# Performance work log

Measured on AMD Instinct MI355X. Metric: run time of the kernel, lower is better.

The kernel has to match this reference:

```python
import jax, jax.numpy as jnp
import numpy as np


def setup_inputs() -> dict:
    key = jax.random.key(0)
    ks = jax.random.split(key, 5)
    B, L, C = 32, 64, 128      # batch, set_size, input_channels
    D, O = 512, 256            # mlp hidden dim, output_channels
    L2 = L * L                 # 4096 = set_size**2 (FSPool set size)
    x = jax.random.normal(ks[0], (B, L, C), dtype=jnp.float32)
    # Linear weights stored as [in, out]; kaiming-ish scaling
    w1 = jax.random.normal(ks[1], (2 * C, D), dtype=jnp.float32) / np.sqrt(2 * C)
    b1 = jnp.zeros((D,), dtype=jnp.float32)
    w2 = jax.random.normal(ks[2], (D, O), dtype=jnp.float32) / np.sqrt(D)
    b2 = jnp.zeros((O,), dtype=jnp.float32)
    # FSPool weight [set_size**2, out_channels], kaiming_normal fan_out linear
    pool_w = jax.random.normal(ks[3], (L2, O), dtype=jnp.float32) / np.sqrt(O)
    return {"x": x, "w1": w1, "b1": b1, "w2": w2, "b2": b2, "pool_w": pool_w}


def reference(x, w1, b1, w2, b2, pool_w):
    B, L, C = x.shape
    # create_pairs + concat: [B, L, L, 2C] -> flatten to [B, L*L, 2C]
    a = jnp.broadcast_to(x[:, :, None, :], (B, L, L, C))
    b = jnp.broadcast_to(x[:, None, :, :], (B, L, L, C))
    pairs = jnp.concatenate([a, b], axis=-1).reshape(B, L * L, 2 * C)
    # 2-layer MLP
    h = jax.nn.relu(pairs @ w1 + b1)            # [B, L^2, D]
    y = h @ w2 + b2                             # [B, L^2, O]
    # FSPool: featurewise sort over set dim, then weighted sum
    y = jnp.sort(y, axis=1)                     # [B, L^2, O]
    return jnp.einsum('nlc,lc->nc', y, pool_w)  # [B, O]
```

## Files before the change

kernel.cpp:

```cpp
#include <hip/hip_runtime.h>
#include <hip/hip_bf16.h>
#include <hip/hip_fp16.h>

typedef __attribute__((ext_vector_type(4))) float f32x4;
typedef _Float16 h8 __attribute__((ext_vector_type(8)));
typedef int i32x4 __attribute__((ext_vector_type(4)));
typedef _Float16 h2 __attribute__((ext_vector_type(2)));

static __device__ __forceinline__ h2 ih2(int x) { return __builtin_bit_cast(h2, x); }
static __device__ __forceinline__ unsigned pkrtz(float lo, float hi) {
  return __builtin_bit_cast(unsigned, __builtin_amdgcn_cvt_pkrtz(lo, hi));
}
static __device__ __forceinline__ int pkmin(int x, int y) {
  int d; asm("v_pk_min_f16 %0, %1, %2" : "=v"(d) : "v"(x), "v"(y)); return d;
}
static __device__ __forceinline__ int pkmax(int x, int y) {
  int d; asm("v_pk_max_f16 %0, %1, %2" : "=v"(d) : "v"(x), "v"(y)); return d;
}
static __device__ __forceinline__ int pkadd(int x, int y) {
  int d; asm("v_pk_add_f16 %0, %1, %2" : "=v"(d) : "v"(x), "v"(y)); return d;
}


__global__ __launch_bounds__(256) void k_uv(const float* __restrict__ x,
                                            const float* __restrict__ w1,
                                            const float* __restrict__ b1,
                                            _Float16* __restrict__ u,
                                            _Float16* __restrict__ v) {
  __shared__ float xs[8 * 128];
  int t = threadIdx.x;
  int r0 = blockIdx.x * 8;
  ((float4*)xs)[t] = ((const float4*)(x + (size_t)r0 * 128))[t];
  __syncthreads();
  int d1 = t, d2 = t + 256;
  float au0[8], au1[8], av0[8], av1[8];
  float bb1 = b1[d1], bb2 = b1[d2];
#pragma unroll
  for (int r = 0; r < 8; ++r) { au0[r] = bb1; au1[r] = bb2; av0[r] = 0.f; av1[r] = 0.f; }
#pragma unroll 4
  for (int c = 0; c < 128; ++c) {
    float wu1 = w1[c * 512 + d1];
    float wu2 = w1[c * 512 + d2];
    float wv1 = w1[(c + 128) * 512 + d1];
    float wv2 = w1[(c + 128) * 512 + d2];
#pragma unroll
    for (int r = 0; r < 8; ++r) {
      float xv = xs[r * 128 + c];
      au0[r] = fmaf(xv, wu1, au0[r]);
      au1[r] = fmaf(xv, wu2, au1[r]);
      av0[r] = fmaf(xv, wv1, av0[r]);
      av1[r] = fmaf(xv, wv2, av1[r]);
    }
  }
#pragma unroll
  for (int r = 0; r < 8; ++r) {
    u[(size_t)(r0 + r) * 512 + d1] = (_Float16)au0[r];
    u[(size_t)(r0 + r) * 512 + d2] = (_Float16)au1[r];
    v[(size_t)(r0 + r) * 512 + d1] = (_Float16)av0[r];
    v[(size_t)(r0 + r) * 512 + d2] = (_Float16)av1[r];
  }
}

__global__ __launch_bounds__(256) void k_w2t(const float* __restrict__ w2,
                                             _Float16* __restrict__ w2t) {
  int n = blockIdx.x;
  int t = threadIdx.x;
  w2t[(size_t)n * 512 + t]       = (_Float16)w2[(size_t)t * 256 + n];
  w2t[(size_t)n * 512 + t + 256] = (_Float16)w2[(size_t)(t + 256) * 256 + n];
}

__global__ __launch_bounds__(256) void k_pwt(const float* __restrict__ pw,
                                             float* __restrict__ pwt) {
  int o = blockIdx.x;
  int t = threadIdx.x;
#pragma unroll
  for (int it = 0; it < 16; ++it) {
    int l = it * 256 + t;
    pwt[(size_t)o * 4096 + l] = pw[(size_t)l * 256 + o];
  }
}

__global__ __launch_bounds__(256, 2) void k_gemm(const _Float16* __restrict__ u,
                                                 const _Float16* __restrict__ v,
                                                 const _Float16* __restrict__ w2t,
                                                 const float* __restrict__ b2,
                                                 unsigned short* __restrict__ yt) {
  __shared__ char vl[64 * 1024];
  __shared__ char ulm[4 * 1024];
  int t = threadIdx.x;
  int n0 = blockIdx.x;
  int bid = (n0 & 7) * 64 + (n0 >> 3);
  int b = bid >> 4, ig = bid & 15;
  {
    const char* vsrc = (const char*)(v + (size_t)b * 64 * 512);
#pragma unroll
    for (int it = 0; it < 16; ++it) {
      int f = it * 4096 + t * 16;
      uint4 d = *(const uint4*)(vsrc + f);
      int row = f >> 10;
      *(uint4*)(vl + (f ^ ((row & 7) << 4))) = d;
    }
    const char* usrc = (const char*)(u + (size_t)(b * 64 + ig * 4) * 512);
    int f = t * 16;
    *(uint4*)(ulm + f) = *(const uint4*)(usrc + f);
  }
  __syncthreads();
  int w = t >> 6, l = t & 63, lr = l & 15, lg = l >> 4;
  const _Float16* bptr[4];
  float bias[4];
#pragma unroll
  for (int ni = 0; ni < 4; ++ni) {
    int col = w * 64 + ni * 16 + lr;
    bptr[ni] = w2t + (size_t)col * 512 + lg * 8;
    bias[ni] = b2[col];
  }
#pragma unroll 1
  for (int ih = 0; ih < 2; ++ih) {
    f32x4 acc[2][4][4];
#pragma unroll
    for (int ip = 0; ip < 2; ++ip)
#pragma unroll
      for (int mi = 0; mi < 4; ++mi)
#pragma unroll
        for (int ni = 0; ni < 4; ++ni) {
          float bv = bias[ni];
          f32x4 ci = {bv, bv, bv, bv};
          acc[ip][mi][ni] = ci;
        }
#pragma unroll 2
    for (int kk = 0; kk < 16; ++kk) {
      h8 bfv[4];
#pragma unroll
      for (int ni = 0; ni < 4; ++ni) bfv[ni] = *(const h8*)(bptr[ni] + kk * 32);
      i32x4 vf[4];
#pragma unroll
      for (int mi = 0; mi < 4; ++mi) {
        int row = mi * 16 + lr;
        int fb = row * 1024 + kk * 64 + lg * 16;
        vf[mi] = *(const i32x4*)(vl + (fb ^ ((row & 7) << 4)));
      }
#pragma unroll
      for (int ip = 0; ip < 2; ++ip) {
        i32x4 uf = *(const i32x4*)(ulm + (ih * 2 + ip) * 1024 + kk * 64 + lg * 16);
#pragma unroll
        for (int mi = 0; mi < 4; ++mi) {
          i32x4 aw;
#pragma unroll
          for (int q = 0; q < 4; ++q) aw[q] = pkmax(pkadd(uf[q], vf[mi][q]), 0);
          h8 af = __builtin_bit_cast(h8, aw);
#pragma unroll
          for (int ni = 0; ni < 4; ++ni)
            acc[ip][mi][ni] =
                __builtin_amdgcn_mfma_f32_16x16x32_f16(af, bfv[ni], acc[ip][mi][ni], 0, 0, 0);
        }
      }
    }
#pragma unroll
    for (int ip = 0; ip < 2; ++ip) {
      int i = ig * 4 + ih * 2 + ip;
#pragma unroll
      for (int ni = 0; ni < 4; ++ni) {
        int col = w * 64 + ni * 16 + lr;
        unsigned short* colbase = yt + (size_t)(b * 256 + col) * 4096 + (size_t)i * 64;
#pragma unroll
        for (int mi = 0; mi < 4; ++mi) {
          f32x4 vv = acc[ip][mi][ni];
          uint2 st;
          st.x = pkrtz(vv[0], vv[1]);
          st.y = pkrtz(vv[2], vv[3]);
          *(uint2*)(colbase + mi * 16 + lg * 4) = st;
        }
      }
    }
  }
}

#define DPP_X1 0xB1
#define DPP_X2 0x4E
#define DPP_X3 0x1B
#define DPP_X7 0x141
#define DPP_X8 0x128
#define DPP_XF 0x140

template <int M, int HB>
static __device__ __forceinline__ void intra(int* a) {
#pragma unroll
  for (int e = 0; e < 64; ++e)
    if ((e & HB) == 0) {
      int f = e ^ M;
      int lo = pkmin(a[e], a[f]);
      int hi = pkmax(a[e], a[f]);
      a[e] = lo;
      a[f] = hi;
    }
}

template <int CTRL>
static __device__ __forceinline__ void cdpp(int* a, bool km) {
#pragma unroll
  for (int e = 0; e < 64; ++e) {
    int r = __builtin_amdgcn_mov_dpp(a[e], CTRL, 0xf, 0xf, true);
    int mn = pkmin(a[e], r), mx = pkmax(a[e], r);
    a[e] = km ? mn : mx;
  }
}

template <int CTRL>
static __device__ __forceinline__ void fdpp(int* a, bool km) {
#pragma unroll
  for (int e = 0; e < 32; ++e) {
    int f = e ^ 63;
    int r0 = __builtin_amdgcn_mov_dpp(a[f], CTRL, 0xf, 0xf, true);
    int r1 = __builtin_amdgcn_mov_dpp(a[e], CTRL, 0xf, 0xf, true);
    int mn0 = pkmin(a[e], r0), mx0 = pkmax(a[e], r0);
    int mn1 = pkmin(a[f], r1), mx1 = pkmax(a[f], r1);
    a[e] = km ? mn0 : mx0;
    a[f] = km ? mn1 : mx1;
  }
}

static __device__ __forceinline__ void cbp(int* a, int tm, bool km, int l) {
  int paddr = ((l ^ tm) & 63) << 2;
#pragma unroll
  for (int e = 0; e < 64; ++e) {
    int r = __builtin_amdgcn_ds_bpermute(paddr, a[e]);
    int mn = pkmin(a[e], r), mx = pkmax(a[e], r);
    a[e] = km ? mn : mx;
  }
}

static __device__ __forceinline__ void fbp(int* a, int tm, bool km, int l) {
  int paddr = ((l ^ tm) & 63) << 2;
#pragma unroll
  for (int e = 0; e < 32; ++e) {
    int f = e ^ 63;
    int r0 = __builtin_amdgcn_ds_bpermute(paddr, a[f]);
    int r1 = __builtin_amdgcn_ds_bpermute(paddr, a[e]);
    int mn0 = pkmin(a[e], r0), mx0 = pkmax(a[e], r0);
    int mn1 = pkmin(a[f], r1), mx1 = pkmax(a[f], r1);
    a[e] = km ? mn0 : mx0;
    a[f] = km ? mn1 : mx1;
  }
}

__global__ __launch_bounds__(64, 2) void k_sortpool(const unsigned short* __restrict__ yt,
                                                    const float* __restrict__ pwt,
                                                    float* __restrict__ out) {
  int t = threadIdx.x;
  int b = blockIdx.x >> 7, p = blockIdx.x & 127;
  int o0 = p * 2, o1 = o0 + 1;
  const uint4* c0 = (const uint4*)(yt + (size_t)(b * 256 + o0) * 4096 + t * 64);
  const uint4* c1 = (const uint4*)(yt + (size_t)(b * 256 + o1) * 4096 + t * 64);
  int a[64];
#pragma unroll
  for (int q = 0; q < 8; ++q) {
    uint4 x0 = c0[q], x1 = c1[q];
    unsigned w0[4] = {x0.x, x0.y, x0.z, x0.w};
    unsigned w1[4] = {x1.x, x1.y, x1.z, x1.w};
#pragma unroll
    for (int r = 0; r < 4; ++r) {
      a[q * 8 + 2 * r]     = (int)((w0[r] & 0xffffu) | (w1[r] << 16));
      a[q * 8 + 2 * r + 1] = (int)((w0[r] >> 16) | (w1[r] & 0xffff0000u));
    }
  }
  intra<1, 1>(a);
  intra<3, 2>(a); intra<1, 1>(a);
  intra<7, 4>(a); intra<2, 2>(a); intra<1, 1>(a);
  intra<15, 8>(a); intra<4, 4>(a); intra<2, 2>(a); intra<1, 1>(a);
  intra<31, 16>(a); intra<8, 8>(a); intra<4, 4>(a); intra<2, 2>(a); intra<1, 1>(a);
  intra<63, 32>(a); intra<16, 16>(a); intra<8, 8>(a); intra<4, 4>(a);
  intra<2, 2>(a); intra<1, 1>(a);
#define CLEAN6 intra<32, 32>(a); intra<16, 16>(a); intra<8, 8>(a); \
               intra<4, 4>(a); intra<2, 2>(a); intra<1, 1>(a)
  fdpp<DPP_X1>(a, !(t & 1)); CLEAN6;
  fdpp<DPP_X3>(a, !(t & 2)); cdpp<DPP_X1>(a, !(t & 1)); CLEAN6;
  fdpp<DPP_X7>(a, !(t & 4)); cdpp<DPP_X2>(a, !(t & 2)); cdpp<DPP_X1>(a, !(t & 1)); CLEAN6;
  fdpp<DPP_XF>(a, !(t & 8)); cbp(a, 4, !(t & 4), t);
  cdpp<DPP_X2>(a, !(t & 2)); cdpp<DPP_X1>(a, !(t & 1)); CLEAN6;
  fbp(a, 31, !(t & 16), t); cdpp<DPP_X8>(a, !(t & 8)); cbp(a, 4, !(t & 4), t);
  cdpp<DPP_X2>(a, !(t & 2)); cdpp<DPP_X1>(a, !(t & 1)); CLEAN6;
  fbp(a, 63, !(t & 32), t); cbp(a, 16, !(t & 16), t); cdpp<DPP_X8>(a, !(t & 8));
  cbp(a, 4, !(t & 4), t); cdpp<DPP_X2>(a, !(t & 2)); cdpp<DPP_X1>(a, !(t & 1)); CLEAN6;
#undef CLEAN6
  const float4* pw0 = (const float4*)(pwt + (size_t)o0 * 4096 + t * 64);
  const float4* pw1 = (const float4*)(pwt + (size_t)o1 * 4096 + t * 64);
  float s0 = 0.f, s1 = 0.f;
#pragma unroll
  for (int q = 0; q < 16; ++q) {
    float4 w0 = pw0[q], w1 = pw1[q];
    float k0[4] = {w0.x, w0.y, w0.z, w0.w};
    float k1[4] = {w1.x, w1.y, w1.z, w1.w};
#pragma unroll
    for (int r = 0; r < 4; ++r) {
      h2 v2 = ih2(a[q * 4 + r]);
      s0 = fmaf((float)v2[0], k0[r], s0);
      s1 = fmaf((float)v2[1], k1[r], s1);
    }
  }
#pragma unroll
  for (int off = 32; off > 0; off >>= 1) {
    s0 += __shfl_xor(s0, off);
    s1 += __shfl_xor(s1, off);
  }
  if (t == 0) {
    out[b * 256 + o0] = s0;
    out[b * 256 + o1] = s1;
  }
}

extern "C" void kernel_launch(void* const* d_in, const int* in_sizes, int n_in,
                              void* d_out, int out_size, void* d_ws, size_t ws_size,
                              hipStream_t stream) {
  const float* x  = (const float*)d_in[0];
  const float* w1 = (const float*)d_in[1];
  const float* b1 = (const float*)d_in[2];
  const float* w2 = (const float*)d_in[3];
  const float* b2 = (const float*)d_in[4];
  const float* pw = (const float*)d_in[5];
  char* ws = (char*)d_ws;
  _Float16* u   = (_Float16*)ws;
  _Float16* v   = (_Float16*)(ws + (2u << 20));
  _Float16* w2t = (_Float16*)(ws + (4u << 20));
  float*    pwt = (float*)(ws + (5u << 20));
  unsigned short* yt = (unsigned short*)(ws + (9u << 20));
  float* out = (float*)d_out;

  k_uv<<<dim3(256), dim3(256), 0, stream>>>(x, w1, b1, u, v);
  k_w2t<<<dim3(256), dim3(256), 0, stream>>>(w2, w2t);
  k_pwt<<<dim3(256), dim3(256), 0, stream>>>(pw, pwt);
  k_gemm<<<dim3(512), dim3(256), 0, stream>>>(u, v, w2t, b2, yt);
  k_sortpool<<<dim3(4096), dim3(64), 0, stream>>>(yt, pwt, out);
}
```

Baseline: 153.3 us.

## Merge prep kernels and cut compare-exchange instruction count in bitonic sort

Folds the three preprocessing kernels (uv projection, w2 transpose, pool-weight transpose) into a single launch that dispatches on block index, removing two kernel launches. The in-register bitonic sort now does each compare-exchange with an xor/max/xor trick (three ops, no separate min) and keeps the cross-lane result with v_bfi on a precomputed lane mask instead of a min, a max and a select. The sortpool launch-bounds min-blocks hint is dropped. Correctness depends on the xor trick and the bfi masks selecting the right halves.

```diff
diff --git a/kernel.cpp b/kernel.cpp
--- a/kernel.cpp
+++ b/kernel.cpp
@@ -11,72 +11,85 @@
 static __device__ __forceinline__ unsigned pkrtz(float lo, float hi) {
   return __builtin_bit_cast(unsigned, __builtin_amdgcn_cvt_pkrtz(lo, hi));
 }
-static __device__ __forceinline__ int pkmin(int x, int y) {
-  int d; asm("v_pk_min_f16 %0, %1, %2" : "=v"(d) : "v"(x), "v"(y)); return d;
-}
-static __device__ __forceinline__ int pkmax(int x, int y) {
+static __device__ __forceinline__ int pkmax_(int x, int y) {
   int d; asm("v_pk_max_f16 %0, %1, %2" : "=v"(d) : "v"(x), "v"(y)); return d;
 }
-static __device__ __forceinline__ int pkadd(int x, int y) {
+static __device__ __forceinline__ int pkadd_(int x, int y) {
   int d; asm("v_pk_add_f16 %0, %1, %2" : "=v"(d) : "v"(x), "v"(y)); return d;
 }
 
-
-__global__ __launch_bounds__(256) void k_uv(const float* __restrict__ x,
-                                            const float* __restrict__ w1,
-                                            const float* __restrict__ b1,
-                                            _Float16* __restrict__ u,
-                                            _Float16* __restrict__ v) {
+static __device__ __forceinline__ void ce(int& x, int& y) {
+  int t;
+  asm("v_xor_b32 %2, %0, %1\n\t"
+      "v_pk_max_f16 %1, %0, %1\n\t"
+      "v_xor_b32 %0, %2, %1"
+      : "+v"(x), "+v"(y), "=&v"(t));
+}
+
+static __device__ __forceinline__ void keep(int& a, int r, int msel) {
+  int mn;
+  asm("v_pk_min_f16 %1, %0, %2\n\t"
+      "v_pk_max_f16 %0, %0, %2\n\t"
+      "v_bfi_b32 %0, %3, %1, %0"
+      : "+v"(a), "=&v"(mn)
+      : "v"(r), "v"(msel));
+}
+
+
+__global__ __launch_bounds__(256) void k_prep(const float* __restrict__ x,
+                                              const float* __restrict__ w1,
+                                              const float* __restrict__ b1,
+                                              const float* __restrict__ w2,
+                                              const float* __restrict__ pw,
+                                              _Float16* __restrict__ u,
+                                              _Float16* __restrict__ v,
+                                              _Float16* __restrict__ w2t,
+                                              float* __restrict__ pwt) {
   __shared__ float xs[8 * 128];
+  int bid = blockIdx.x;
   int t = threadIdx.x;
-  int r0 = blockIdx.x * 8;
-  ((float4*)xs)[t] = ((const float4*)(x + (size_t)r0 * 128))[t];
-  __syncthreads();
-  int d1 = t, d2 = t + 256;
-  float au0[8], au1[8], av0[8], av1[8];
-  float bb1 = b1[d1], bb2 = b1[d2];
-#pragma unroll
-  for (int r = 0; r < 8; ++r) { au0[r] = bb1; au1[r] = bb2; av0[r] = 0.f; av1[r] = 0.f; }
+  if (bid < 256) {
+    int r0 = bid * 8;
+    ((float4*)xs)[t] = ((const float4*)(x + (size_t)r0 * 128))[t];
+    __syncthreads();
+    int d1 = t, d2 = t + 256;
+    float au0[8], au1[8], av0[8], av1[8];
+    float bb1 = b1[d1], bb2 = b1[d2];
+#pragma unroll
+    for (int r = 0; r < 8; ++r) { au0[r] = bb1; au1[r] = bb2; av0[r] = 0.f; av1[r] = 0.f; }
 #pragma unroll 4
-  for (int c = 0; c < 128; ++c) {
-    float wu1 = w1[c * 512 + d1];
-    float wu2 = w1[c * 512 + d2];
-    float wv1 = w1[(c + 128) * 512 + d1];
-    float wv2 = w1[(c + 128) * 512 + d2];
+    for (int c = 0; c < 128; ++c) {
+      float wu1 = w1[c * 512 + d1];
+      float wu2 = w1[c * 512 + d2];
+      float wv1 = w1[(c + 128) * 512 + d1];
+      float wv2 = w1[(c + 128) * 512 + d2];
+#pragma unroll
+      for (int r = 0; r < 8; ++r) {
+        float xv = xs[r * 128 + c];
+        au0[r] = fmaf(xv, wu1, au0[r]);
+        au1[r] = fmaf(xv, wu2, au1[r]);
+        av0[r] = fmaf(xv, wv1, av0[r]);
+        av1[r] = fmaf(xv, wv2, av1[r]);
+      }
+    }
 #pragma unroll
     for (int r = 0; r < 8; ++r) {
-      float xv = xs[r * 128 + c];
-      au0[r] = fmaf(xv, wu1, au0[r]);
-      au1[r] = fmaf(xv, wu2, au1[r]);
-      av0[r] = fmaf(xv, wv1, av0[r]);
-      av1[r] = fmaf(xv, wv2, av1[r]);
-    }
-  }
-#pragma unroll
-  for (int r = 0; r < 8; ++r) {
-    u[(size_t)(r0 + r) * 512 + d1] = (_Float16)au0[r];
-    u[(size_t)(r0 + r) * 512 + d2] = (_Float16)au1[r];
-    v[(size_t)(r0 + r) * 512 + d1] = (_Float16)av0[r];
-    v[(size_t)(r0 + r) * 512 + d2] = (_Float16)av1[r];
-  }
-}
-
-__global__ __launch_bounds__(256) void k_w2t(const float* __restrict__ w2,
-                                             _Float16* __restrict__ w2t) {
-  int n = blockIdx.x;
-  int t = threadIdx.x;
-  w2t[(size_t)n * 512 + t]       = (_Float16)w2[(size_t)t * 256 + n];
-  w2t[(size_t)n * 512 + t + 256] = (_Float16)w2[(size_t)(t + 256) * 256 + n];
-}
-
-__global__ __launch_bounds__(256) void k_pwt(const float* __restrict__ pw,
-                                             float* __restrict__ pwt) {
-  int o = blockIdx.x;
-  int t = threadIdx.x;
-#pragma unroll
-  for (int it = 0; it < 16; ++it) {
-    int l = it * 256 + t;
-    pwt[(size_t)o * 4096 + l] = pw[(size_t)l * 256 + o];
+      u[(size_t)(r0 + r) * 512 + d1] = (_Float16)au0[r];
+      u[(size_t)(r0 + r) * 512 + d2] = (_Float16)au1[r];
+      v[(size_t)(r0 + r) * 512 + d1] = (_Float16)av0[r];
+      v[(size_t)(r0 + r) * 512 + d2] = (_Float16)av1[r];
+    }
+  } else if (bid < 512) {
+    int n = bid - 256;
+    w2t[(size_t)n * 512 + t]       = (_Float16)w2[(size_t)t * 256 + n];
+    w2t[(size_t)n * 512 + t + 256] = (_Float16)w2[(size_t)(t + 256) * 256 + n];
+  } else {
+    int o = bid - 512;
+#pragma unroll
+    for (int it = 0; it < 16; ++it) {
+      int l = it * 256 + t;
+      pwt[(size_t)o * 4096 + l] = pw[(size_t)l * 256 + o];
+    }
   }
 }
 
@@ -146,7 +159,7 @@
         for (int mi = 0; mi < 4; ++mi) {
           i32x4 aw;
 #pragma unroll
-          for (int q = 0; q < 4; ++q) aw[q] = pkmax(pkadd(uf[q], vf[mi][q]), 0);
+          for (int q = 0; q < 4; ++q) aw[q] = pkmax_(pkadd_(uf[q], vf[mi][q]), 0);
           h8 af = __builtin_bit_cast(h8, aw);
 #pragma unroll
           for (int ni = 0; ni < 4; ++ni)
@@ -186,66 +199,54 @@
 static __device__ __forceinline__ void intra(int* a) {
 #pragma unroll
   for (int e = 0; e < 64; ++e)
-    if ((e & HB) == 0) {
-      int f = e ^ M;
-      int lo = pkmin(a[e], a[f]);
-      int hi = pkmax(a[e], a[f]);
-      a[e] = lo;
-      a[f] = hi;
-    }
+    if ((e & HB) == 0) ce(a[e], a[e ^ M]);
 }
 
 template <int CTRL>
-static __device__ __forceinline__ void cdpp(int* a, bool km) {
+static __device__ __forceinline__ void cdpp(int* a, int msel) {
 #pragma unroll
   for (int e = 0; e < 64; ++e) {
     int r = __builtin_amdgcn_mov_dpp(a[e], CTRL, 0xf, 0xf, true);
-    int mn = pkmin(a[e], r), mx = pkmax(a[e], r);
-    a[e] = km ? mn : mx;
+    keep(a[e], r, msel);
   }
 }
 
 template <int CTRL>
-static __device__ __forceinline__ void fdpp(int* a, bool km) {
+static __device__ __forceinline__ void fdpp(int* a, int msel) {
 #pragma unroll
   for (int e = 0; e < 32; ++e) {
     int f = e ^ 63;
     int r0 = __builtin_amdgcn_mov_dpp(a[f], CTRL, 0xf, 0xf, true);
     int r1 = __builtin_amdgcn_mov_dpp(a[e], CTRL, 0xf, 0xf, true);
-    int mn0 = pkmin(a[e], r0), mx0 = pkmax(a[e], r0);
-    int mn1 = pkmin(a[f], r1), mx1 = pkmax(a[f], r1);
-    a[e] = km ? mn0 : mx0;
-    a[f] = km ? mn1 : mx1;
-  }
-}
-
-static __device__ __forceinline__ void cbp(int* a, int tm, bool km, int l) {
+    keep(a[e], r0, msel);
+    keep(a[f], r1, msel);
+  }
+}
+
+static __device__ __forceinline__ void cbp(int* a, int tm, int msel, int l) {
   int paddr = ((l ^ tm) & 63) << 2;
 #pragma unroll
   for (int e = 0; e < 64; ++e) {
     int r = __builtin_amdgcn_ds_bpermute(paddr, a[e]);
-    int mn = pkmin(a[e], r), mx = pkmax(a[e], r);
-    a[e] = km ? mn : mx;
-  }
-}
-
-static __device__ __forceinline__ void fbp(int* a, int tm, bool km, int l) {
+    keep(a[e], r, msel);
+  }
+}
+
+static __device__ __forceinline__ void fbp(int* a, int tm, int msel, int l) {
   int paddr = ((l ^ tm) & 63) << 2;
 #pragma unroll
   for (int e = 0; e < 32; ++e) {
     int f = e ^ 63;
     int r0 = __builtin_amdgcn_ds_bpermute(paddr, a[f]);
     int r1 = __builtin_amdgcn_ds_bpermute(paddr, a[e]);
-    int mn0 = pkmin(a[e], r0), mx0 = pkmax(a[e], r0);
-    int mn1 = pkmin(a[f], r1), mx1 = pkmax(a[f], r1);
-    a[e] = km ? mn0 : mx0;
-    a[f] = km ? mn1 : mx1;
-  }
-}
-
-__global__ __launch_bounds__(64, 2) void k_sortpool(const unsigned short* __restrict__ yt,
-                                                    const float* __restrict__ pwt,
-                                                    float* __restrict__ out) {
+    keep(a[e], r0, msel);
+    keep(a[f], r1, msel);
+  }
+}
+
+__global__ __launch_bounds__(64) void k_sortpool(const unsigned short* __restrict__ yt,
+                                                 const float* __restrict__ pwt,
+                                                 float* __restrict__ out) {
   int t = threadIdx.x;
   int b = blockIdx.x >> 7, p = blockIdx.x & 127;
   int o0 = p * 2, o1 = o0 + 1;
@@ -263,6 +264,12 @@
       a[q * 8 + 2 * r + 1] = (int)((w0[r] >> 16) | (w1[r] & 0xffff0000u));
     }
   }
+  int m1  = (t & 1)  ? 0 : -1;
+  int m2  = (t & 2)  ? 0 : -1;
+  int m4  = (t & 4)  ? 0 : -1;
+  int m8  = (t & 8)  ? 0 : -1;
+  int m16 = (t & 16) ? 0 : -1;
+  int m32 = (t & 32) ? 0 : -1;
   intra<1, 1>(a);
   intra<3, 2>(a); intra<1, 1>(a);
   intra<7, 4>(a); intra<2, 2>(a); intra<1, 1>(a);
@@ -272,15 +279,15 @@
   intra<2, 2>(a); intra<1, 1>(a);
 #define CLEAN6 intra<32, 32>(a); intra<16, 16>(a); intra<8, 8>(a); \
                intra<4, 4>(a); intra<2, 2>(a); intra<1, 1>(a)
-  fdpp<DPP_X1>(a, !(t & 1)); CLEAN6;
-  fdpp<DPP_X3>(a, !(t & 2)); cdpp<DPP_X1>(a, !(t & 1)); CLEAN6;
-  fdpp<DPP_X7>(a, !(t & 4)); cdpp<DPP_X2>(a, !(t & 2)); cdpp<DPP_X1>(a, !(t & 1)); CLEAN6;
-  fdpp<DPP_XF>(a, !(t & 8)); cbp(a, 4, !(t & 4), t);
-  cdpp<DPP_X2>(a, !(t & 2)); cdpp<DPP_X1>(a, !(t & 1)); CLEAN6;
-  fbp(a, 31, !(t & 16), t); cdpp<DPP_X8>(a, !(t & 8)); cbp(a, 4, !(t & 4), t);
-  cdpp<DPP_X2>(a, !(t & 2)); cdpp<DPP_X1>(a, !(t & 1)); CLEAN6;
-  fbp(a, 63, !(t & 32), t); cbp(a, 16, !(t & 16), t); cdpp<DPP_X8>(a, !(t & 8));
-  cbp(a, 4, !(t & 4), t); cdpp<DPP_X2>(a, !(t & 2)); cdpp<DPP_X1>(a, !(t & 1)); CLEAN6;
+  fdpp<DPP_X1>(a, m1); CLEAN6;
+  fdpp<DPP_X3>(a, m2); cdpp<DPP_X1>(a, m1); CLEAN6;
+  fdpp<DPP_X7>(a, m4); cdpp<DPP_X2>(a, m2); cdpp<DPP_X1>(a, m1); CLEAN6;
+  fdpp<DPP_XF>(a, m8); cbp(a, 4, m4, t);
+  cdpp<DPP_X2>(a, m2); cdpp<DPP_X1>(a, m1); CLEAN6;
+  fbp(a, 31, m16, t); cdpp<DPP_X8>(a, m8); cbp(a, 4, m4, t);
+  cdpp<DPP_X2>(a, m2); cdpp<DPP_X1>(a, m1); CLEAN6;
+  fbp(a, 63, m32, t); cbp(a, 16, m16, t); cdpp<DPP_X8>(a, m8);
+  cbp(a, 4, m4, t); cdpp<DPP_X2>(a, m2); cdpp<DPP_X1>(a, m1); CLEAN6;
 #undef CLEAN6
   const float4* pw0 = (const float4*)(pwt + (size_t)o0 * 4096 + t * 64);
   const float4* pw1 = (const float4*)(pwt + (size_t)o1 * 4096 + t * 64);
@@ -325,9 +332,7 @@
   unsigned short* yt = (unsigned short*)(ws + (9u << 20));
   float* out = (float*)d_out;
 
-  k_uv<<<dim3(256), dim3(256), 0, stream>>>(x, w1, b1, u, v);
-  k_w2t<<<dim3(256), dim3(256), 0, stream>>>(w2, w2t);
-  k_pwt<<<dim3(256), dim3(256), 0, stream>>>(pw, pwt);
+  k_prep<<<dim3(768), dim3(256), 0, stream>>>(x, w1, b1, w2, pw, u, v, w2t, pwt);
   k_gemm<<<dim3(512), dim3(256), 0, stream>>>(u, v, w2t, b2, yt);
   k_sortpool<<<dim3(4096), dim3(64), 0, stream>>>(yt, pwt, out);
 }
```

Result: no change. 151.0 us (-1.6%).

## Merge prep kernels and split GEMM into one-row blocks with wider N tiles

Applied to the files above, without the earlier changes.

Fuses the three preprocessing kernels (u/v projection, w2 transpose, pool weight transpose) into one launch, dispatching on block index. Reworks the GEMM so each block handles a single i row: four waves split into 2 j-halves by 2 n-halves, each holding 2x8 MFMA tiles, with 2048 blocks instead of 512. This adds parallelism and removes two launches, at the cost of reloading the 64KB v tile from global memory four times as often. Also drops the occupancy hint of 2 from the sortpool launch bounds.

```diff
diff --git a/kernel.cpp b/kernel.cpp
--- a/kernel.cpp
+++ b/kernel.cpp
@@ -22,61 +22,60 @@
 }
 
 
-__global__ __launch_bounds__(256) void k_uv(const float* __restrict__ x,
-                                            const float* __restrict__ w1,
-                                            const float* __restrict__ b1,
-                                            _Float16* __restrict__ u,
-                                            _Float16* __restrict__ v) {
+__global__ __launch_bounds__(256) void k_prep(const float* __restrict__ x,
+                                              const float* __restrict__ w1,
+                                              const float* __restrict__ b1,
+                                              const float* __restrict__ w2,
+                                              const float* __restrict__ pw,
+                                              _Float16* __restrict__ u,
+                                              _Float16* __restrict__ v,
+                                              _Float16* __restrict__ w2t,
+                                              float* __restrict__ pwt) {
   __shared__ float xs[8 * 128];
+  int bid = blockIdx.x;
   int t = threadIdx.x;
-  int r0 = blockIdx.x * 8;
-  ((float4*)xs)[t] = ((const float4*)(x + (size_t)r0 * 128))[t];
-  __syncthreads();
-  int d1 = t, d2 = t + 256;
-  float au0[8], au1[8], av0[8], av1[8];
-  float bb1 = b1[d1], bb2 = b1[d2];
-#pragma unroll
-  for (int r = 0; r < 8; ++r) { au0[r] = bb1; au1[r] = bb2; av0[r] = 0.f; av1[r] = 0.f; }
+  if (bid < 256) {
+    int r0 = bid * 8;
+    ((float4*)xs)[t] = ((const float4*)(x + (size_t)r0 * 128))[t];
+    __syncthreads();
+    int d1 = t, d2 = t + 256;
+    float au0[8], au1[8], av0[8], av1[8];
+    float bb1 = b1[d1], bb2 = b1[d2];
+#pragma unroll
+    for (int r = 0; r < 8; ++r) { au0[r] = bb1; au1[r] = bb2; av0[r] = 0.f; av1[r] = 0.f; }
 #pragma unroll 4
-  for (int c = 0; c < 128; ++c) {
-    float wu1 = w1[c * 512 + d1];
-    float wu2 = w1[c * 512 + d2];
-    float wv1 = w1[(c + 128) * 512 + d1];
-    float wv2 = w1[(c + 128) * 512 + d2];
+    for (int c = 0; c < 128; ++c) {
+      float wu1 = w1[c * 512 + d1];
+      float wu2 = w1[c * 512 + d2];
+      float wv1 = w1[(c + 128) * 512 + d1];
+      float wv2 = w1[(c + 128) * 512 + d2];
+#pragma unroll
+      for (int r = 0; r < 8; ++r) {
+        float xv = xs[r * 128 + c];
+        au0[r] = fmaf(xv, wu1, au0[r]);
+        au1[r] = fmaf(xv, wu2, au1[r]);
+        av0[r] = fmaf(xv, wv1, av0[r]);
+        av1[r] = fmaf(xv, wv2, av1[r]);
+      }
+    }
 #pragma unroll
     for (int r = 0; r < 8; ++r) {
-      float xv = xs[r * 128 + c];
-      au0[r] = fmaf(xv, wu1, au0[r]);
-      au1[r] = fmaf(xv, wu2, au1[r]);
-      av0[r] = fmaf(xv, wv1, av0[r]);
-      av1[r] = fmaf(xv, wv2, av1[r]);
-    }
-  }
-#pragma unroll
-  for (int r = 0; r < 8; ++r) {
-    u[(size_t)(r0 + r) * 512 + d1] = (_Float16)au0[r];
-    u[(size_t)(r0 + r) * 512 + d2] = (_Float16)au1[r];
-    v[(size_t)(r0 + r) * 512 + d1] = (_Float16)av0[r];
-    v[(size_t)(r0 + r) * 512 + d2] = (_Float16)av1[r];
-  }
-}
-
-__global__ __launch_bounds__(256) void k_w2t(const float* __restrict__ w2,
-                                             _Float16* __restrict__ w2t) {
-  int n = blockIdx.x;
-  int t = threadIdx.x;
-  w2t[(size_t)n * 512 + t]       = (_Float16)w2[(size_t)t * 256 + n];
-  w2t[(size_t)n * 512 + t + 256] = (_Float16)w2[(size_t)(t + 256) * 256 + n];
-}
-
-__global__ __launch_bounds__(256) void k_pwt(const float* __restrict__ pw,
-                                             float* __restrict__ pwt) {
-  int o = blockIdx.x;
-  int t = threadIdx.x;
-#pragma unroll
-  for (int it = 0; it < 16; ++it) {
-    int l = it * 256 + t;
-    pwt[(size_t)o * 4096 + l] = pw[(size_t)l * 256 + o];
+      u[(size_t)(r0 + r) * 512 + d1] = (_Float16)au0[r];
+      u[(size_t)(r0 + r) * 512 + d2] = (_Float16)au1[r];
+      v[(size_t)(r0 + r) * 512 + d1] = (_Float16)av0[r];
+      v[(size_t)(r0 + r) * 512 + d2] = (_Float16)av1[r];
+    }
+  } else if (bid < 512) {
+    int n = bid - 256;
+    w2t[(size_t)n * 512 + t]       = (_Float16)w2[(size_t)t * 256 + n];
+    w2t[(size_t)n * 512 + t + 256] = (_Float16)w2[(size_t)(t + 256) * 256 + n];
+  } else {
+    int o = bid - 512;
+#pragma unroll
+    for (int it = 0; it < 16; ++it) {
+      int l = it * 256 + t;
+      pwt[(size_t)o * 4096 + l] = pw[(size_t)l * 256 + o];
+    }
   }
 }
 
@@ -86,11 +85,11 @@
                                                  const float* __restrict__ b2,
                                                  unsigned short* __restrict__ yt) {
   __shared__ char vl[64 * 1024];
-  __shared__ char ulm[4 * 1024];
+  __shared__ char ulm[1024];
   int t = threadIdx.x;
   int n0 = blockIdx.x;
-  int bid = (n0 & 7) * 64 + (n0 >> 3);
-  int b = bid >> 4, ig = bid & 15;
+  int bid = (n0 & 7) * 256 + (n0 >> 3);
+  int b = bid >> 6, i = bid & 63;
   {
     const char* vsrc = (const char*)(v + (size_t)b * 64 * 512);
 #pragma unroll
@@ -100,79 +99,61 @@
       int row = f >> 10;
       *(uint4*)(vl + (f ^ ((row & 7) << 4))) = d;
     }
-    const char* usrc = (const char*)(u + (size_t)(b * 64 + ig * 4) * 512);
-    int f = t * 16;
-    *(uint4*)(ulm + f) = *(const uint4*)(usrc + f);
+    if (t < 64) {
+      const char* usrc = (const char*)(u + (size_t)(b * 64 + i) * 512);
+      *(uint4*)(ulm + t * 16) = *(const uint4*)(usrc + t * 16);
+    }
   }
   __syncthreads();
   int w = t >> 6, l = t & 63, lr = l & 15, lg = l >> 4;
-  const _Float16* bptr[4];
-  float bias[4];
-#pragma unroll
-  for (int ni = 0; ni < 4; ++ni) {
-    int col = w * 64 + ni * 16 + lr;
+  int jh = w & 1, nh = w >> 1;
+  const _Float16* bptr[8];
+  f32x4 acc[2][8];
+#pragma unroll
+  for (int ni = 0; ni < 8; ++ni) {
+    int col = nh * 128 + ni * 16 + lr;
     bptr[ni] = w2t + (size_t)col * 512 + lg * 8;
-    bias[ni] = b2[col];
-  }
-#pragma unroll 1
-  for (int ih = 0; ih < 2; ++ih) {
-    f32x4 acc[2][4][4];
-#pragma unroll
-    for (int ip = 0; ip < 2; ++ip)
-#pragma unroll
-      for (int mi = 0; mi < 4; ++mi)
-#pragma unroll
-        for (int ni = 0; ni < 4; ++ni) {
-          float bv = bias[ni];
-          f32x4 ci = {bv, bv, bv, bv};
-          acc[ip][mi][ni] = ci;
-        }
-#pragma unroll 2
-    for (int kk = 0; kk < 16; ++kk) {
-      h8 bfv[4];
-#pragma unroll
-      for (int ni = 0; ni < 4; ++ni) bfv[ni] = *(const h8*)(bptr[ni] + kk * 32);
-      i32x4 vf[4];
-#pragma unroll
-      for (int mi = 0; mi < 4; ++mi) {
-        int row = mi * 16 + lr;
-        int fb = row * 1024 + kk * 64 + lg * 16;
-        vf[mi] = *(const i32x4*)(vl + (fb ^ ((row & 7) << 4)));
-      }
-#pragma unroll
-      for (int ip = 0; ip < 2; ++ip) {
-        i32x4 uf = *(const i32x4*)(ulm + (ih * 2 + ip) * 1024 + kk * 64 + lg * 16);
-#pragma unroll
-        for (int mi = 0; mi < 4; ++mi) {
-          i32x4 aw;
-#pragma unroll
-          for (int q = 0; q < 4; ++q) aw[q] = pkmax(pkadd(uf[q], vf[mi][q]), 0);
-          h8 af = __builtin_bit_cast(h8, aw);
-#pragma unroll
-          for (int ni = 0; ni < 4; ++ni)
-            acc[ip][mi][ni] =
-                __builtin_amdgcn_mfma_f32_16x16x32_f16(af, bfv[ni], acc[ip][mi][ni], 0, 0, 0);
-        }
-      }
-    }
-#pragma unroll
-    for (int ip = 0; ip < 2; ++ip) {
-      int i = ig * 4 + ih * 2 + ip;
-#pragma unroll
-      for (int ni = 0; ni < 4; ++ni) {
-        int col = w * 64 + ni * 16 + lr;
-        unsigned short* colbase = yt + (size_t)(b * 256 + col) * 4096 + (size_t)i * 64;
-#pragma unroll
-        for (int mi = 0; mi < 4; ++mi) {
-          f32x4 vv = acc[ip][mi][ni];
-          uint2 st;
-          st.x = pkrtz(vv[0], vv[1]);
-          st.y = pkrtz(vv[2], vv[3]);
-          *(uint2*)(colbase + mi * 16 + lg * 4) = st;
-        }
-      }
-    }
-  }
+    float bv = b2[col];
+    f32x4 ci = {bv, bv, bv, bv};
+    acc[0][ni] = ci;
+    acc[1][ni] = ci;
+  }
+#pragma unroll 4
+  for (int kk = 0; kk < 16; ++kk) {
+    h8 bfv[8];
+#pragma unroll
+    for (int ni = 0; ni < 8; ++ni) bfv[ni] = *(const h8*)(bptr[ni] + kk * 32);
+    i32x4 uf = *(const i32x4*)(ulm + kk * 64 + lg * 16);
+    h8 af[2];
+#pragma unroll
+    for (int mi = 0; mi < 2; ++mi) {
+      int row = jh * 32 + mi * 16 + lr;
+      int fb = row * 1024 + kk * 64 + lg * 16;
+      i32x4 vf = *(const i32x4*)(vl + (fb ^ ((row & 7) << 4)));
+      i32x4 aw;
+#pragma unroll
+      for (int q = 0; q < 4; ++q) aw[q] = pkmax(pkadd(uf[q], vf[q]), 0);
+      af[mi] = __builtin_bit_cast(h8, aw);
+    }
+#pragma unroll
+    for (int mi = 0; mi < 2; ++mi)
+#pragma unroll
+      for (int ni = 0; ni < 8; ++ni)
+        acc[mi][ni] = __builtin_amdgcn_mfma_f32_16x16x32_f16(af[mi], bfv[ni], acc[mi][ni], 0, 0, 0);
+  }
+#pragma unroll
+  for (int mi = 0; mi < 2; ++mi)
+#pragma unroll
+    for (int ni = 0; ni < 8; ++ni) {
+      int col = nh * 128 + ni * 16 + lr;
+      unsigned short* colbase =
+          yt + (size_t)(b * 256 + col) * 4096 + (size_t)i * 64 + jh * 32 + mi * 16 + lg * 4;
+      f32x4 vv = acc[mi][ni];
+      uint2 st;
+      st.x = pkrtz(vv[0], vv[1]);
+      st.y = pkrtz(vv[2], vv[3]);
+      *(uint2*)colbase = st;
+    }
 }
 
 #define DPP_X1 0xB1
@@ -243,9 +224,9 @@
   }
 }
 
-__global__ __launch_bounds__(64, 2) void k_sortpool(const unsigned short* __restrict__ yt,
-                                                    const float* __restrict__ pwt,
-                                                    float* __restrict__ out) {
+__global__ __launch_bounds__(64) void k_sortpool(const unsigned short* __restrict__ yt,
+                                                 const float* __restrict__ pwt,
+                                                 float* __restrict__ out) {
   int t = threadIdx.x;
   int b = blockIdx.x >> 7, p = blockIdx.x & 127;
   int o0 = p * 2, o1 = o0 + 1;
@@ -325,9 +306,7 @@
   unsigned short* yt = (unsigned short*)(ws + (9u << 20));
   float* out = (float*)d_out;
 
-  k_uv<<<dim3(256), dim3(256), 0, stream>>>(x, w1, b1, u, v);
-  k_w2t<<<dim3(256), dim3(256), 0, stream>>>(w2, w2t);
-  k_pwt<<<dim3(256), dim3(256), 0, stream>>>(pw, pwt);
-  k_gemm<<<dim3(512), dim3(256), 0, stream>>>(u, v, w2t, b2, yt);
+  k_prep<<<dim3(768), dim3(256), 0, stream>>>(x, w1, b1, w2, pw, u, v, w2t, pwt);
+  k_gemm<<<dim3(2048), dim3(256), 0, stream>>>(u, v, w2t, b2, yt);
   k_sortpool<<<dim3(4096), dim3(64), 0, stream>>>(yt, pwt, out);
 }
```

Measured after the change: 229.7 us. +49.8%, slower.

## Merge prep kernels into one launch and split GEMM tiles across j halves

Applied to the files above, without the earlier changes.

The three preprocessing kernels (u/v projection, w2 transpose, pool-weight transpose) are merged into one launch that dispatches on block index, removing two kernel launches and their serialization gaps. The GEMM grid doubles to 1024 blocks, each handling half of the 64 j-rows, so the v tile in LDS shrinks to 32 KB and the accumulator set halves. The aim is more blocks per CU and better occupancy, at the cost of loading w2t B-fragments twice as often overall. The sortpool launch bound drops its min-blocks hint, which loosens the register cap.

```diff
diff --git a/kernel.cpp b/kernel.cpp
--- a/kernel.cpp
+++ b/kernel.cpp
@@ -22,61 +22,60 @@
 }
 
 
-__global__ __launch_bounds__(256) void k_uv(const float* __restrict__ x,
-                                            const float* __restrict__ w1,
-                                            const float* __restrict__ b1,
-                                            _Float16* __restrict__ u,
-                                            _Float16* __restrict__ v) {
+__global__ __launch_bounds__(256) void k_prep(const float* __restrict__ x,
+                                              const float* __restrict__ w1,
+                                              const float* __restrict__ b1,
+                                              const float* __restrict__ w2,
+                                              const float* __restrict__ pw,
+                                              _Float16* __restrict__ u,
+                                              _Float16* __restrict__ v,
+                                              _Float16* __restrict__ w2t,
+                                              float* __restrict__ pwt) {
   __shared__ float xs[8 * 128];
+  int bid = blockIdx.x;
   int t = threadIdx.x;
-  int r0 = blockIdx.x * 8;
-  ((float4*)xs)[t] = ((const float4*)(x + (size_t)r0 * 128))[t];
-  __syncthreads();
-  int d1 = t, d2 = t + 256;
-  float au0[8], au1[8], av0[8], av1[8];
-  float bb1 = b1[d1], bb2 = b1[d2];
-#pragma unroll
-  for (int r = 0; r < 8; ++r) { au0[r] = bb1; au1[r] = bb2; av0[r] = 0.f; av1[r] = 0.f; }
+  if (bid < 256) {
+    int r0 = bid * 8;
+    ((float4*)xs)[t] = ((const float4*)(x + (size_t)r0 * 128))[t];
+    __syncthreads();
+    int d1 = t, d2 = t + 256;
+    float au0[8], au1[8], av0[8], av1[8];
+    float bb1 = b1[d1], bb2 = b1[d2];
+#pragma unroll
+    for (int r = 0; r < 8; ++r) { au0[r] = bb1; au1[r] = bb2; av0[r] = 0.f; av1[r] = 0.f; }
 #pragma unroll 4
-  for (int c = 0; c < 128; ++c) {
-    float wu1 = w1[c * 512 + d1];
-    float wu2 = w1[c * 512 + d2];
-    float wv1 = w1[(c + 128) * 512 + d1];
-    float wv2 = w1[(c + 128) * 512 + d2];
+    for (int c = 0; c < 128; ++c) {
+      float wu1 = w1[c * 512 + d1];
+      float wu2 = w1[c * 512 + d2];
+      float wv1 = w1[(c + 128) * 512 + d1];
+      float wv2 = w1[(c + 128) * 512 + d2];
+#pragma unroll
+      for (int r = 0; r < 8; ++r) {
+        float xv = xs[r * 128 + c];
+        au0[r] = fmaf(xv, wu1, au0[r]);
+        au1[r] = fmaf(xv, wu2, au1[r]);
+        av0[r] = fmaf(xv, wv1, av0[r]);
+        av1[r] = fmaf(xv, wv2, av1[r]);
+      }
+    }
 #pragma unroll
     for (int r = 0; r < 8; ++r) {
-      float xv = xs[r * 128 + c];
-      au0[r] = fmaf(xv, wu1, au0[r]);
-      au1[r] = fmaf(xv, wu2, au1[r]);
-      av0[r] = fmaf(xv, wv1, av0[r]);
-      av1[r] = fmaf(xv, wv2, av1[r]);
-    }
-  }
-#pragma unroll
-  for (int r = 0; r < 8; ++r) {
-    u[(size_t)(r0 + r) * 512 + d1] = (_Float16)au0[r];
-    u[(size_t)(r0 + r) * 512 + d2] = (_Float16)au1[r];
-    v[(size_t)(r0 + r) * 512 + d1] = (_Float16)av0[r];
-    v[(size_t)(r0 + r) * 512 + d2] = (_Float16)av1[r];
-  }
-}
-
-__global__ __launch_bounds__(256) void k_w2t(const float* __restrict__ w2,
-                                             _Float16* __restrict__ w2t) {
-  int n = blockIdx.x;
-  int t = threadIdx.x;
-  w2t[(size_t)n * 512 + t]       = (_Float16)w2[(size_t)t * 256 + n];
-  w2t[(size_t)n * 512 + t + 256] = (_Float16)w2[(size_t)(t + 256) * 256 + n];
-}
-
-__global__ __launch_bounds__(256) void k_pwt(const float* __restrict__ pw,
-                                             float* __restrict__ pwt) {
-  int o = blockIdx.x;
-  int t = threadIdx.x;
-#pragma unroll
-  for (int it = 0; it < 16; ++it) {
-    int l = it * 256 + t;
-    pwt[(size_t)o * 4096 + l] = pw[(size_t)l * 256 + o];
+      u[(size_t)(r0 + r) * 512 + d1] = (_Float16)au0[r];
+      u[(size_t)(r0 + r) * 512 + d2] = (_Float16)au1[r];
+      v[(size_t)(r0 + r) * 512 + d1] = (_Float16)av0[r];
+      v[(size_t)(r0 + r) * 512 + d2] = (_Float16)av1[r];
+    }
+  } else if (bid < 512) {
+    int n = bid - 256;
+    w2t[(size_t)n * 512 + t]       = (_Float16)w2[(size_t)t * 256 + n];
+    w2t[(size_t)n * 512 + t + 256] = (_Float16)w2[(size_t)(t + 256) * 256 + n];
+  } else {
+    int o = bid - 512;
+#pragma unroll
+    for (int it = 0; it < 16; ++it) {
+      int l = it * 256 + t;
+      pwt[(size_t)o * 4096 + l] = pw[(size_t)l * 256 + o];
+    }
   }
 }
 
@@ -85,24 +84,24 @@
                                                  const _Float16* __restrict__ w2t,
                                                  const float* __restrict__ b2,
                                                  unsigned short* __restrict__ yt) {
-  __shared__ char vl[64 * 1024];
+  __shared__ char vl[32 * 1024];
   __shared__ char ulm[4 * 1024];
   int t = threadIdx.x;
   int n0 = blockIdx.x;
-  int bid = (n0 & 7) * 64 + (n0 >> 3);
-  int b = bid >> 4, ig = bid & 15;
+  int bid = (n0 & 7) * 128 + (n0 >> 3);
+  int b = bid >> 5, rest = bid & 31;
+  int ig = rest >> 1, jh = rest & 1;
   {
-    const char* vsrc = (const char*)(v + (size_t)b * 64 * 512);
-#pragma unroll
-    for (int it = 0; it < 16; ++it) {
+    const char* vsrc = (const char*)(v + (size_t)(b * 64 + jh * 32) * 512);
+#pragma unroll
+    for (int it = 0; it < 8; ++it) {
       int f = it * 4096 + t * 16;
       uint4 d = *(const uint4*)(vsrc + f);
       int row = f >> 10;
       *(uint4*)(vl + (f ^ ((row & 7) << 4))) = d;
     }
     const char* usrc = (const char*)(u + (size_t)(b * 64 + ig * 4) * 512);
-    int f = t * 16;
-    *(uint4*)(ulm + f) = *(const uint4*)(usrc + f);
+    *(uint4*)(ulm + t * 16) = *(const uint4*)(usrc + t * 16);
   }
   __syncthreads();
   int w = t >> 6, l = t & 63, lr = l & 15, lg = l >> 4;
@@ -116,11 +115,11 @@
   }
 #pragma unroll 1
   for (int ih = 0; ih < 2; ++ih) {
-    f32x4 acc[2][4][4];
+    f32x4 acc[2][2][4];
 #pragma unroll
     for (int ip = 0; ip < 2; ++ip)
 #pragma unroll
-      for (int mi = 0; mi < 4; ++mi)
+      for (int mi = 0; mi < 2; ++mi)
 #pragma unroll
         for (int ni = 0; ni < 4; ++ni) {
           float bv = bias[ni];
@@ -132,9 +131,9 @@
       h8 bfv[4];
 #pragma unroll
       for (int ni = 0; ni < 4; ++ni) bfv[ni] = *(const h8*)(bptr[ni] + kk * 32);
-      i32x4 vf[4];
-#pragma unroll
-      for (int mi = 0; mi < 4; ++mi) {
+      i32x4 vf[2];
+#pragma unroll
+      for (int mi = 0; mi < 2; ++mi) {
         int row = mi * 16 + lr;
         int fb = row * 1024 + kk * 64 + lg * 16;
         vf[mi] = *(const i32x4*)(vl + (fb ^ ((row & 7) << 4)));
@@ -143,7 +142,7 @@
       for (int ip = 0; ip < 2; ++ip) {
         i32x4 uf = *(const i32x4*)(ulm + (ih * 2 + ip) * 1024 + kk * 64 + lg * 16);
 #pragma unroll
-        for (int mi = 0; mi < 4; ++mi) {
+        for (int mi = 0; mi < 2; ++mi) {
           i32x4 aw;
 #pragma unroll
           for (int q = 0; q < 4; ++q) aw[q] = pkmax(pkadd(uf[q], vf[mi][q]), 0);
@@ -159,18 +158,18 @@
     for (int ip = 0; ip < 2; ++ip) {
       int i = ig * 4 + ih * 2 + ip;
 #pragma unroll
-      for (int ni = 0; ni < 4; ++ni) {
-        int col = w * 64 + ni * 16 + lr;
-        unsigned short* colbase = yt + (size_t)(b * 256 + col) * 4096 + (size_t)i * 64;
-#pragma unroll
-        for (int mi = 0; mi < 4; ++mi) {
+      for (int mi = 0; mi < 2; ++mi)
+#pragma unroll
+        for (int ni = 0; ni < 4; ++ni) {
+          int col = w * 64 + ni * 16 + lr;
+          unsigned short* colbase =
+              yt + (size_t)(b * 256 + col) * 4096 + (size_t)i * 64 + jh * 32 + mi * 16 + lg * 4;
           f32x4 vv = acc[ip][mi][ni];
           uint2 st;
           st.x = pkrtz(vv[0], vv[1]);
           st.y = pkrtz(vv[2], vv[3]);
-          *(uint2*)(colbase + mi * 16 + lg * 4) = st;
+          *(uint2*)colbase = st;
         }
-      }
     }
   }
 }
@@ -243,9 +242,9 @@
   }
 }
 
-__global__ __launch_bounds__(64, 2) void k_sortpool(const unsigned short* __restrict__ yt,
-                                                    const float* __restrict__ pwt,
-                                                    float* __restrict__ out) {
+__global__ __launch_bounds__(64) void k_sortpool(const unsigned short* __restrict__ yt,
+                                                 const float* __restrict__ pwt,
+                                                 float* __restrict__ out) {
   int t = threadIdx.x;
   int b = blockIdx.x >> 7, p = blockIdx.x & 127;
   int o0 = p * 2, o1 = o0 + 1;
@@ -325,9 +324,7 @@
   unsigned short* yt = (unsigned short*)(ws + (9u << 20));
   float* out = (float*)d_out;
 
-  k_uv<<<dim3(256), dim3(256), 0, stream>>>(x, w1, b1, u, v);
-  k_w2t<<<dim3(256), dim3(256), 0, stream>>>(w2, w2t);
-  k_pwt<<<dim3(256), dim3(256), 0, stream>>>(pw, pwt);
-  k_gemm<<<dim3(512), dim3(256), 0, stream>>>(u, v, w2t, b2, yt);
+  k_prep<<<dim3(768), dim3(256), 0, stream>>>(x, w1, b1, w2, pw, u, v, w2t, pwt);
+  k_gemm<<<dim3(1024), dim3(256), 0, stream>>>(u, v, w2t, b2, yt);
   k_sortpool<<<dim3(4096), dim3(64), 0, stream>>>(yt, pwt, out);
 }
```

Measured after the change: 171.3 us. +11.7%, slower.
